# Kernel optimization log

Hardware: AMD Instinct MI355X
Metric: run time of the kernel (lower is better)

The kernel has to match this reference:

```python
import jax, jax.numpy as jnp
import numpy as np

EMB = 768
HS = 64
B, T = 4, 4096


def setup_inputs() -> dict:
    key = jax.random.key(0)
    ks = jax.random.split(key, 7)
    s = 1.0 / np.sqrt(EMB)
    return {
        "x": jax.random.normal(ks[0], (B, T, EMB), dtype=jnp.float32),
        "Wk": jax.random.normal(ks[1], (EMB, HS), dtype=jnp.float32) * s,
        "bk": jnp.zeros((HS,), dtype=jnp.float32),
        "Wq": jax.random.normal(ks[2], (EMB, HS), dtype=jnp.float32) * s,
        "bq": jnp.zeros((HS,), dtype=jnp.float32),
        "Wv": jax.random.normal(ks[3], (EMB, HS), dtype=jnp.float32) * s,
        "bv": jnp.zeros((HS,), dtype=jnp.float32),
    }


def reference(x, Wk, bk, Wq, bq, Wv, bv):
    # Linear projections: (B, T, emb) @ (emb, hs) + bias -> (B, T, hs)
    k = x @ Wk + bk
    q = x @ Wq + bq
    v = x @ Wv + bv
    # NOTE: original code computes key @ query^T (k on the left), no 1/sqrt(hs) scaling.
    att = jnp.einsum("bth,bsh->bts", k, q)  # (B, T, T)
    causal = jnp.tril(jnp.ones((T, T), dtype=bool))  # (T, T)
    att = jnp.where(causal, att, -jnp.inf)
    wei = jax.nn.softmax(att, axis=-1)
    return jnp.einsum("bts,bsh->bth", wei, v)  # (B, T, hs)
```

## Files before the change

kernel.cpp:

```cpp
#include <hip/hip_runtime.h>
#include <cmath>

static constexpr int EMB  = 768;
static constexpr int HS   = 64;
static constexpr int NB   = 4;
static constexpr int SEQ  = 4096;
static constexpr int MTOT = NB * SEQ;
static constexpr int SPLITS = 8;

typedef __attribute__((ext_vector_type(8))) short  short8x;
typedef __attribute__((ext_vector_type(4))) float  float4x;
typedef __attribute__((ext_vector_type(4))) unsigned short ushort4x;

__device__ inline unsigned short rne16(float f) {
    unsigned u = __builtin_bit_cast(unsigned, f);
    unsigned r = u + 0x7FFFu + ((u >> 16) & 1u);
    return (unsigned short)(r >> 16);
}
__device__ inline float bf2f(unsigned short h) {
    return __builtin_bit_cast(float, ((unsigned)h) << 16);
}

__global__ __launch_bounds__(256) void convert_w(
    const float* __restrict__ Wk, const float* __restrict__ Wq, const float* __restrict__ Wv,
    unsigned short* __restrict__ wpk)
{
    const int t    = blockIdx.x * 256 + threadIdx.x;
    const int lane = t & 63;
    const int rest = t >> 6;
    const int nng  = rest % 12;
    const int kcp  = rest / 12;
    const int kc   = kcp % 24;
    const int p    = kcp / 24;
    const int which= nng >> 2;
    const int nn   = nng & 3;
    const float* W = (which == 0) ? Wk : (which == 1) ? Wq : Wv;
    const int col  = nn * 16 + (lane & 15);
    const int kr   = kc * 32 + (lane >> 4) * 8;

    unsigned short o[8];
    #pragma unroll
    for (int j = 0; j < 8; ++j) {
        float w = W[(size_t)(kr + j) * HS + col];
        unsigned short h = rne16(w);
        o[j] = (p == 0) ? h : rne16(w - bf2f(h));
    }
    size_t base = ((size_t)((p * 24 + kc) * 12 + nng) * 64 + lane) * 8;
    *(short8x*)&wpk[base] = *(short8x*)o;
}

__global__ __launch_bounds__(256) void proj_kernel(
    const float* __restrict__ x,
    const unsigned short* __restrict__ wpk,
    const float* __restrict__ bk, const float* __restrict__ bq, const float* __restrict__ bv,
    unsigned short* __restrict__ khi, unsigned short* __restrict__ klo,
    unsigned short* __restrict__ qhi, unsigned short* __restrict__ qlo,
    unsigned short* __restrict__ vT)
{
    __shared__ unsigned short xh[2][32 * 72];
    __shared__ unsigned short xl[2][32 * 72];

    const int tid  = threadIdx.x;
    const int lane = tid & 63;
    const int w    = tid >> 6;
    const int l15  = lane & 15;
    const int quad = lane >> 4;
    const int row0 = blockIdx.x * 32;

    float4x acc[3][2] = {};
    float4  pre[2];

    #pragma unroll
    for (int it = 0; it < 2; ++it) {
        const int fi = tid + it * 256;
        const int r  = fi >> 4, c4 = (fi & 15) * 4;
        pre[it] = *(const float4*)&x[(size_t)(row0 + r) * EMB + 0 * 64 + c4];
    }
    #pragma unroll
    for (int it = 0; it < 2; ++it) {
        const int fi = tid + it * 256;
        const int r  = fi >> 4, c4 = (fi & 15) * 4;
        const float4 xv = pre[it];
        const unsigned short h0 = rne16(xv.x), h1 = rne16(xv.y),
                             h2 = rne16(xv.z), h3 = rne16(xv.w);
        ushort4x hv = {h0, h1, h2, h3};
        ushort4x lv = {rne16(xv.x - bf2f(h0)), rne16(xv.y - bf2f(h1)),
                       rne16(xv.z - bf2f(h2)), rne16(xv.w - bf2f(h3))};
        *(ushort4x*)&xh[0][r * 72 + c4] = hv;
        *(ushort4x*)&xl[0][r * 72 + c4] = lv;
    }

    for (int ch = 0; ch < 12; ++ch) {
        if (ch + 1 < 12) {
            #pragma unroll
            for (int it = 0; it < 2; ++it) {
                const int fi = tid + it * 256;
                const int r  = fi >> 4, c4 = (fi & 15) * 4;
                pre[it] = *(const float4*)&x[(size_t)(row0 + r) * EMB + (ch + 1) * 64 + c4];
            }
        }
        __syncthreads();
        const int buf = ch & 1;

        #pragma unroll
        for (int k0i = 0; k0i < 2; ++k0i) {
            const int k0 = k0i * 32;
            const int kc = ch * 2 + k0i;
            short8x ah[2], al[2];
            #pragma unroll
            for (int mi = 0; mi < 2; ++mi) {
                ah[mi] = *(const short8x*)&xh[buf][(mi * 16 + l15) * 72 + k0 + quad * 8];
                al[mi] = *(const short8x*)&xl[buf][(mi * 16 + l15) * 72 + k0 + quad * 8];
            }
            #pragma unroll
            for (int which = 0; which < 3; ++which) {
                const int nng = which * 4 + w;
                const short8x bh = *(const short8x*)&wpk[((size_t)((0 * 24 + kc) * 12 + nng) * 64 + lane) * 8];
                const short8x bl = *(const short8x*)&wpk[((size_t)((1 * 24 + kc) * 12 + nng) * 64 + lane) * 8];
                #pragma unroll
                for (int mi = 0; mi < 2; ++mi) {
                    acc[which][mi] = __builtin_amdgcn_mfma_f32_16x16x32_bf16(ah[mi], bh, acc[which][mi], 0, 0, 0);
                    acc[which][mi] = __builtin_amdgcn_mfma_f32_16x16x32_bf16(ah[mi], bl, acc[which][mi], 0, 0, 0);
                    acc[which][mi] = __builtin_amdgcn_mfma_f32_16x16x32_bf16(al[mi], bh, acc[which][mi], 0, 0, 0);
                }
            }
        }

        if (ch + 1 < 12) {
            const int nbuf = (ch + 1) & 1;
            #pragma unroll
            for (int it = 0; it < 2; ++it) {
                const int fi = tid + it * 256;
                const int r  = fi >> 4, c4 = (fi & 15) * 4;
                const float4 xv = pre[it];
                const unsigned short h0 = rne16(xv.x), h1 = rne16(xv.y),
                                     h2 = rne16(xv.z), h3 = rne16(xv.w);
                ushort4x hv = {h0, h1, h2, h3};
                ushort4x lv = {rne16(xv.x - bf2f(h0)), rne16(xv.y - bf2f(h1)),
                               rne16(xv.z - bf2f(h2)), rne16(xv.w - bf2f(h3))};
                *(ushort4x*)&xh[nbuf][r * 72 + c4] = hv;
                *(ushort4x*)&xl[nbuf][r * 72 + c4] = lv;
            }
        }
    }

    const int col = w * 16 + l15;
    const float bkv = bk[col], bqv = bq[col], bvv = bv[col];
    #pragma unroll
    for (int mi = 0; mi < 2; ++mi) {
        const int rbase = row0 + mi * 16 + quad * 4;
        #pragma unroll
        for (int r = 0; r < 4; ++r) {
            const float kv = acc[0][mi][r] + bkv;
            const unsigned short hk = rne16(kv);
            khi[(size_t)(rbase + r) * 64 + col] = hk;
            klo[(size_t)(rbase + r) * 64 + col] = rne16(kv - bf2f(hk));
            const float qv = acc[1][mi][r] + bqv;
            const unsigned short hq = rne16(qv);
            qhi[(size_t)(rbase + r) * 64 + col] = hq;
            qlo[(size_t)(rbase + r) * 64 + col] = rne16(qv - bf2f(hq));
        }
        const int b = rbase / SEQ;
        const int s = rbase % SEQ;
        ushort4x vv = {rne16(acc[2][mi][0] + bvv), rne16(acc[2][mi][1] + bvv),
                       rne16(acc[2][mi][2] + bvv), rne16(acc[2][mi][3] + bvv)};
        *(ushort4x*)&vT[((size_t)b * 64 + col) * SEQ + s] = vv;
    }
}

__global__ __launch_bounds__(256, 2) void attn_kernel(
    const unsigned short* __restrict__ khi, const unsigned short* __restrict__ klo,
    const unsigned short* __restrict__ qhi, const unsigned short* __restrict__ qlo,
    const unsigned short* __restrict__ vT,
    float* __restrict__ Opart, float* __restrict__ lpart)
{
    __shared__ unsigned short qh_s[64 * 72];
    __shared__ unsigned short ql_s[64 * 72];
    __shared__ unsigned short vt_s[64 * 72];
    __shared__ unsigned short psH[64 * 72];
    __shared__ unsigned short psL[64 * 72];

    const int tid  = threadIdx.x;
    const int lane = tid & 63;
    const int w    = tid >> 6;
    const int l15  = lane & 15;
    const int quad = lane >> 4;

    const int n  = blockIdx.x;
    const int sp = n & (SPLITS - 1);
    const int b  = (n >> 3) & (NB - 1);
    const int p  = n >> 5;
    const int jj[4] = {63 - p, 32 + p, 31 - p, p};
    const size_t rowb = (size_t)b * SEQ;

    float4x oacc[4][4] = {};
    float   l_r[4][4]  = {};

    const int sr = tid >> 3;
    const int c8 = (tid & 7) * 8;

    for (int ci = sp; ci <= jj[0]; ci += SPLITS) {
        const int s0 = ci * 64;
        __syncthreads();
        #pragma unroll
        for (int it = 0; it < 2; ++it) {
            const int r = sr + it * 32;
            *(short8x*)&qh_s[r * 72 + c8] = *(const short8x*)&qhi[(rowb + s0 + r) * 64 + c8];
            *(short8x*)&ql_s[r * 72 + c8] = *(const short8x*)&qlo[(rowb + s0 + r) * 64 + c8];
            *(short8x*)&vt_s[r * 72 + c8] = *(const short8x*)&vT[((size_t)b * 64 + r) * SEQ + s0 + c8];
        }
        __syncthreads();

        #pragma unroll
        for (int g = 0; g < 2; ++g) {
            const int idxH = g ? 1 : 0;
            const int idxL = g ? 2 : 3;
            const int jH = jj[idxH], jL = jj[idxL];
            const bool aH = (ci <= jH), aL = (ci <= jL);
            if (!aH && !aL) continue;

            short8x ahH[2], alH[2], ahL[2], alL[2];
            #pragma unroll
            for (int k0 = 0; k0 < 2; ++k0) {
                if (aH) {
                    const size_t rH = (rowb + jH * 64 + 16 * w + l15) * 64 + k0 * 32 + quad * 8;
                    ahH[k0] = *(const short8x*)&khi[rH];
                    alH[k0] = *(const short8x*)&klo[rH];
                }
                if (aL) {
                    const size_t rL = (rowb + jL * 64 + 16 * w + l15) * 64 + k0 * 32 + quad * 8;
                    ahL[k0] = *(const short8x*)&khi[rL];
                    alL[k0] = *(const short8x*)&klo[rL];
                }
            }

            float4x sH[4] = {}, sL[4] = {};
            #pragma unroll
            for (int k0 = 0; k0 < 2; ++k0) {
                #pragma unroll
                for (int nn = 0; nn < 4; ++nn) {
                    const short8x bh = *(const short8x*)&qh_s[(nn * 16 + l15) * 72 + k0 * 32 + quad * 8];
                    const short8x bl = *(const short8x*)&ql_s[(nn * 16 + l15) * 72 + k0 * 32 + quad * 8];
                    if (aH) {
                        sH[nn] = __builtin_amdgcn_mfma_f32_16x16x32_bf16(ahH[k0], bh, sH[nn], 0, 0, 0);
                        sH[nn] = __builtin_amdgcn_mfma_f32_16x16x32_bf16(alH[k0], bh, sH[nn], 0, 0, 0);
                        sH[nn] = __builtin_amdgcn_mfma_f32_16x16x32_bf16(ahH[k0], bl, sH[nn], 0, 0, 0);
                    }
                    if (aL) {
                        sL[nn] = __builtin_amdgcn_mfma_f32_16x16x32_bf16(ahL[k0], bh, sL[nn], 0, 0, 0);
                        sL[nn] = __builtin_amdgcn_mfma_f32_16x16x32_bf16(alL[k0], bh, sL[nn], 0, 0, 0);
                        sL[nn] = __builtin_amdgcn_mfma_f32_16x16x32_bf16(ahL[k0], bl, sL[nn], 0, 0, 0);
                    }
                }
            }

            #pragma unroll
            for (int hl = 0; hl < 2; ++hl) {
                const bool alive = hl ? aL : aH;
                if (!alive) continue;
                const int j   = hl ? jL : jH;
                const int idx = hl ? idxL : idxH;
                float4x* sc   = hl ? sL : sH;
                unsigned short* ps = hl ? psL : psH;
                if (ci == j) {
                    const int trow = j * 64 + 16 * w + quad * 4;
                    #pragma unroll
                    for (int nn = 0; nn < 4; ++nn) {
                        const int colg = s0 + nn * 16 + l15;
                        #pragma unroll
                        for (int r = 0; r < 4; ++r)
                            if (colg > trow + r) sc[nn][r] = -1e30f;
                    }
                }
                #pragma unroll
                for (int nn = 0; nn < 4; ++nn) {
                    #pragma unroll
                    for (int r = 0; r < 4; ++r) {
                        const float e = __expf(fminf(sc[nn][r], 80.0f));
                        const unsigned short h = rne16(e);
                        l_r[idx][r] += bf2f(h);
                        ps[(16 * w + quad * 4 + r) * 72 + nn * 16 + l15] = h;
                    }
                }
            }

            #pragma unroll
            for (int k0 = 0; k0 < 2; ++k0) {
                short8x paH, paL;
                if (aH) paH = *(const short8x*)&psH[(16 * w + l15) * 72 + k0 * 32 + quad * 8];
                if (aL) paL = *(const short8x*)&psL[(16 * w + l15) * 72 + k0 * 32 + quad * 8];
                #pragma unroll
                for (int nn = 0; nn < 4; ++nn) {
                    const short8x vb = *(const short8x*)&vt_s[(nn * 16 + l15) * 72 + k0 * 32 + quad * 8];
                    if (aH) oacc[idxH][nn] = __builtin_amdgcn_mfma_f32_16x16x32_bf16(paH, vb, oacc[idxH][nn], 0, 0, 0);
                    if (aL) oacc[idxL][nn] = __builtin_amdgcn_mfma_f32_16x16x32_bf16(paL, vb, oacc[idxL][nn], 0, 0, 0);
                }
            }
        }
    }

    #pragma unroll
    for (int idx = 0; idx < 4; ++idx) {
        const int j = jj[idx];
        if (idx == 3 && sp > p) continue;
        float lv[4];
        #pragma unroll
        for (int r = 0; r < 4; ++r) {
            float l = l_r[idx][r];
            l += __shfl_xor(l, 1);
            l += __shfl_xor(l, 2);
            l += __shfl_xor(l, 4);
            l += __shfl_xor(l, 8);
            lv[r] = l;
        }
        const size_t part = (size_t)(j * NB + b) * SPLITS + sp;
        float* Op = Opart + part * 4096;
        #pragma unroll
        for (int nn = 0; nn < 4; ++nn)
            #pragma unroll
            for (int r = 0; r < 4; ++r)
                Op[(16 * w + quad * 4 + r) * 64 + nn * 16 + l15] = oacc[idx][nn][r];
        if (l15 == 0) {
            #pragma unroll
            for (int r = 0; r < 4; ++r)
                lpart[part * 64 + 16 * w + quad * 4 + r] = lv[r];
        }
    }
}

__global__ __launch_bounds__(256) void combine_kernel(
    const float* __restrict__ Opart, const float* __restrict__ lpart,
    float* __restrict__ out)
{
    const int j   = blockIdx.x;
    const int b   = blockIdx.y;
    const int tid = threadIdx.x;
    const int row = tid >> 2;
    const int c0  = (tid & 3) * 16;
    const size_t base = (size_t)(j * NB + b) * SPLITS;

    float4 acc[4] = {};
    float lsum = 0.f;
    for (int sp = 0; sp < SPLITS; ++sp) {
        const float l = lpart[(base + sp) * 64 + row];
        if (l > 0.f) {
            lsum += l;
            const float* Op = Opart + (base + sp) * 4096 + row * 64 + c0;
            #pragma unroll
            for (int u = 0; u < 4; ++u) {
                const float4 v = *(const float4*)&Op[u * 4];
                acc[u].x += v.x; acc[u].y += v.y; acc[u].z += v.z; acc[u].w += v.w;
            }
        }
    }
    const float inv = 1.0f / lsum;
    float* o = out + ((size_t)b * SEQ + j * 64 + row) * 64 + c0;
    #pragma unroll
    for (int u = 0; u < 4; ++u) {
        float4 v;
        v.x = acc[u].x * inv; v.y = acc[u].y * inv;
        v.z = acc[u].z * inv; v.w = acc[u].w * inv;
        *(float4*)&o[u * 4] = v;
    }
}

extern "C" void kernel_launch(void* const* d_in, const int* in_sizes, int n_in,
                              void* d_out, int out_size, void* d_ws, size_t ws_size,
                              hipStream_t stream)
{
    const float* x  = (const float*)d_in[0];
    const float* Wk = (const float*)d_in[1];
    const float* bk = (const float*)d_in[2];
    const float* Wq = (const float*)d_in[3];
    const float* bq = (const float*)d_in[4];
    const float* Wv = (const float*)d_in[5];
    const float* bv = (const float*)d_in[6];
    float* out = (float*)d_out;

    const size_t NE = (size_t)MTOT * HS;
    unsigned short* khi = (unsigned short*)d_ws;
    unsigned short* klo = khi + NE;
    unsigned short* qhi = klo + NE;
    unsigned short* qlo = qhi + NE;
    unsigned short* vT  = qlo + NE;
    unsigned short* wpk = vT + NE;
    float* Opart = (float*)(wpk + 294912);
    float* lpart = Opart + (size_t)64 * NB * SPLITS * 4096;

    hipMemsetAsync(lpart, 0, (size_t)64 * NB * SPLITS * 64 * sizeof(float), stream);
    convert_w<<<144, 256, 0, stream>>>(Wk, Wq, Wv, wpk);
    proj_kernel<<<MTOT / 32, 256, 0, stream>>>(x, wpk, bk, bq, bv, khi, klo, qhi, qlo, vT);
    attn_kernel<<<16 * NB * SPLITS, 256, 0, stream>>>(khi, klo, qhi, qlo, vT, Opart, lpart);
    dim3 cgrid(64, NB);
    combine_kernel<<<cgrid, 256, 0, stream>>>(Opart, lpart, out);
}
```

Baseline: 160.6 us.

## Raise attention split count, store normalized bf16 partials, shrink projection tiles

The attention kernel now uses a runtime split count, 16 by default and dropping to 8 if the workspace is too small, doubling the grid to improve load balance and occupancy across CUs. Partial outputs are normalized per split and stored as bf16, halving partial-output traffic. The combine kernel reweights them by each split's l. The two P staging buffers merge into one to cut LDS and allow 4 blocks per CU, and the projection kernel uses 16-row tiles with doubled grid. Storing partials in bf16 costs output precision, and more splits add combine work.

After: 224.9 us. 1.4x slower.

```diff
diff --git a/kernel.cpp b/kernel.cpp
--- a/kernel.cpp
+++ b/kernel.cpp
@@ -6,7 +6,6 @@
 static constexpr int NB   = 4;
 static constexpr int SEQ  = 4096;
 static constexpr int MTOT = NB * SEQ;
-static constexpr int SPLITS = 8;
 
 typedef __attribute__((ext_vector_type(8))) short  short8x;
 typedef __attribute__((ext_vector_type(4))) float  float4x;
@@ -49,7 +48,7 @@
     *(short8x*)&wpk[base] = *(short8x*)o;
 }
 
-__global__ __launch_bounds__(256) void proj_kernel(
+__global__ __launch_bounds__(256, 4) void proj_kernel(
     const float* __restrict__ x,
     const unsigned short* __restrict__ wpk,
     const float* __restrict__ bk, const float* __restrict__ bq, const float* __restrict__ bv,
@@ -57,48 +56,37 @@
     unsigned short* __restrict__ qhi, unsigned short* __restrict__ qlo,
     unsigned short* __restrict__ vT)
 {
-    __shared__ unsigned short xh[2][32 * 72];
-    __shared__ unsigned short xl[2][32 * 72];
+    __shared__ unsigned short xh[2][16 * 72];
+    __shared__ unsigned short xl[2][16 * 72];
 
     const int tid  = threadIdx.x;
     const int lane = tid & 63;
     const int w    = tid >> 6;
     const int l15  = lane & 15;
     const int quad = lane >> 4;
-    const int row0 = blockIdx.x * 32;
-
-    float4x acc[3][2] = {};
-    float4  pre[2];
-
-    #pragma unroll
-    for (int it = 0; it < 2; ++it) {
-        const int fi = tid + it * 256;
-        const int r  = fi >> 4, c4 = (fi & 15) * 4;
-        pre[it] = *(const float4*)&x[(size_t)(row0 + r) * EMB + 0 * 64 + c4];
-    }
-    #pragma unroll
-    for (int it = 0; it < 2; ++it) {
-        const int fi = tid + it * 256;
-        const int r  = fi >> 4, c4 = (fi & 15) * 4;
-        const float4 xv = pre[it];
+    const int row0 = blockIdx.x * 16;
+
+    const int s_r  = tid >> 4;
+    const int s_c4 = (tid & 15) * 4;
+
+    float4x acc[3] = {};
+    float4  pre;
+
+    pre = *(const float4*)&x[(size_t)(row0 + s_r) * EMB + 0 * 64 + s_c4];
+    {
+        const float4 xv = pre;
         const unsigned short h0 = rne16(xv.x), h1 = rne16(xv.y),
                              h2 = rne16(xv.z), h3 = rne16(xv.w);
         ushort4x hv = {h0, h1, h2, h3};
         ushort4x lv = {rne16(xv.x - bf2f(h0)), rne16(xv.y - bf2f(h1)),
                        rne16(xv.z - bf2f(h2)), rne16(xv.w - bf2f(h3))};
-        *(ushort4x*)&xh[0][r * 72 + c4] = hv;
-        *(ushort4x*)&xl[0][r * 72 + c4] = lv;
+        *(ushort4x*)&xh[0][s_r * 72 + s_c4] = hv;
+        *(ushort4x*)&xl[0][s_r * 72 + s_c4] = lv;
     }
 
     for (int ch = 0; ch < 12; ++ch) {
-        if (ch + 1 < 12) {
-            #pragma unroll
-            for (int it = 0; it < 2; ++it) {
-                const int fi = tid + it * 256;
-                const int r  = fi >> 4, c4 = (fi & 15) * 4;
-                pre[it] = *(const float4*)&x[(size_t)(row0 + r) * EMB + (ch + 1) * 64 + c4];
-            }
-        }
+        if (ch + 1 < 12)
+            pre = *(const float4*)&x[(size_t)(row0 + s_r) * EMB + (ch + 1) * 64 + s_c4];
         __syncthreads();
         const int buf = ch & 1;
 
@@ -106,79 +94,63 @@
         for (int k0i = 0; k0i < 2; ++k0i) {
             const int k0 = k0i * 32;
             const int kc = ch * 2 + k0i;
-            short8x ah[2], al[2];
-            #pragma unroll
-            for (int mi = 0; mi < 2; ++mi) {
-                ah[mi] = *(const short8x*)&xh[buf][(mi * 16 + l15) * 72 + k0 + quad * 8];
-                al[mi] = *(const short8x*)&xl[buf][(mi * 16 + l15) * 72 + k0 + quad * 8];
-            }
+            const short8x ah = *(const short8x*)&xh[buf][l15 * 72 + k0 + quad * 8];
+            const short8x al = *(const short8x*)&xl[buf][l15 * 72 + k0 + quad * 8];
             #pragma unroll
             for (int which = 0; which < 3; ++which) {
                 const int nng = which * 4 + w;
                 const short8x bh = *(const short8x*)&wpk[((size_t)((0 * 24 + kc) * 12 + nng) * 64 + lane) * 8];
                 const short8x bl = *(const short8x*)&wpk[((size_t)((1 * 24 + kc) * 12 + nng) * 64 + lane) * 8];
-                #pragma unroll
-                for (int mi = 0; mi < 2; ++mi) {
-                    acc[which][mi] = __builtin_amdgcn_mfma_f32_16x16x32_bf16(ah[mi], bh, acc[which][mi], 0, 0, 0);
-                    acc[which][mi] = __builtin_amdgcn_mfma_f32_16x16x32_bf16(ah[mi], bl, acc[which][mi], 0, 0, 0);
-                    acc[which][mi] = __builtin_amdgcn_mfma_f32_16x16x32_bf16(al[mi], bh, acc[which][mi], 0, 0, 0);
-                }
+                acc[which] = __builtin_amdgcn_mfma_f32_16x16x32_bf16(ah, bh, acc[which], 0, 0, 0);
+                acc[which] = __builtin_amdgcn_mfma_f32_16x16x32_bf16(ah, bl, acc[which], 0, 0, 0);
+                acc[which] = __builtin_amdgcn_mfma_f32_16x16x32_bf16(al, bh, acc[which], 0, 0, 0);
             }
         }
 
         if (ch + 1 < 12) {
             const int nbuf = (ch + 1) & 1;
-            #pragma unroll
-            for (int it = 0; it < 2; ++it) {
-                const int fi = tid + it * 256;
-                const int r  = fi >> 4, c4 = (fi & 15) * 4;
-                const float4 xv = pre[it];
-                const unsigned short h0 = rne16(xv.x), h1 = rne16(xv.y),
-                                     h2 = rne16(xv.z), h3 = rne16(xv.w);
-                ushort4x hv = {h0, h1, h2, h3};
-                ushort4x lv = {rne16(xv.x - bf2f(h0)), rne16(xv.y - bf2f(h1)),
-                               rne16(xv.z - bf2f(h2)), rne16(xv.w - bf2f(h3))};
-                *(ushort4x*)&xh[nbuf][r * 72 + c4] = hv;
-                *(ushort4x*)&xl[nbuf][r * 72 + c4] = lv;
-            }
+            const float4 xv = pre;
+            const unsigned short h0 = rne16(xv.x), h1 = rne16(xv.y),
+                                 h2 = rne16(xv.z), h3 = rne16(xv.w);
+            ushort4x hv = {h0, h1, h2, h3};
+            ushort4x lv = {rne16(xv.x - bf2f(h0)), rne16(xv.y - bf2f(h1)),
+                           rne16(xv.z - bf2f(h2)), rne16(xv.w - bf2f(h3))};
+            *(ushort4x*)&xh[nbuf][s_r * 72 + s_c4] = hv;
+            *(ushort4x*)&xl[nbuf][s_r * 72 + s_c4] = lv;
         }
     }
 
     const int col = w * 16 + l15;
     const float bkv = bk[col], bqv = bq[col], bvv = bv[col];
+    const int rbase = row0 + quad * 4;
     #pragma unroll
-    for (int mi = 0; mi < 2; ++mi) {
-        const int rbase = row0 + mi * 16 + quad * 4;
-        #pragma unroll
-        for (int r = 0; r < 4; ++r) {
-            const float kv = acc[0][mi][r] + bkv;
-            const unsigned short hk = rne16(kv);
-            khi[(size_t)(rbase + r) * 64 + col] = hk;
-            klo[(size_t)(rbase + r) * 64 + col] = rne16(kv - bf2f(hk));
-            const float qv = acc[1][mi][r] + bqv;
-            const unsigned short hq = rne16(qv);
-            qhi[(size_t)(rbase + r) * 64 + col] = hq;
-            qlo[(size_t)(rbase + r) * 64 + col] = rne16(qv - bf2f(hq));
-        }
-        const int b = rbase / SEQ;
-        const int s = rbase % SEQ;
-        ushort4x vv = {rne16(acc[2][mi][0] + bvv), rne16(acc[2][mi][1] + bvv),
-                       rne16(acc[2][mi][2] + bvv), rne16(acc[2][mi][3] + bvv)};
-        *(ushort4x*)&vT[((size_t)b * 64 + col) * SEQ + s] = vv;
-    }
-}
-
-__global__ __launch_bounds__(256, 2) void attn_kernel(
+    for (int r = 0; r < 4; ++r) {
+        const float kv = acc[0][r] + bkv;
+        const unsigned short hk = rne16(kv);
+        khi[(size_t)(rbase + r) * 64 + col] = hk;
+        klo[(size_t)(rbase + r) * 64 + col] = rne16(kv - bf2f(hk));
+        const float qv = acc[1][r] + bqv;
+        const unsigned short hq = rne16(qv);
+        qhi[(size_t)(rbase + r) * 64 + col] = hq;
+        qlo[(size_t)(rbase + r) * 64 + col] = rne16(qv - bf2f(hq));
+    }
+    const int b = rbase / SEQ;
+    const int s = rbase % SEQ;
+    ushort4x vv = {rne16(acc[2][0] + bvv), rne16(acc[2][1] + bvv),
+                   rne16(acc[2][2] + bvv), rne16(acc[2][3] + bvv)};
+    *(ushort4x*)&vT[((size_t)b * 64 + col) * SEQ + s] = vv;
+}
+
+__global__ __launch_bounds__(256, 4) void attn_kernel(
     const unsigned short* __restrict__ khi, const unsigned short* __restrict__ klo,
     const unsigned short* __restrict__ qhi, const unsigned short* __restrict__ qlo,
     const unsigned short* __restrict__ vT,
-    float* __restrict__ Opart, float* __restrict__ lpart)
+    unsigned short* __restrict__ Opart, float* __restrict__ lpart, int S)
 {
     __shared__ unsigned short qh_s[64 * 72];
     __shared__ unsigned short ql_s[64 * 72];
     __shared__ unsigned short vt_s[64 * 72];
-    __shared__ unsigned short psH[64 * 72];
-    __shared__ unsigned short psL[64 * 72];
+    __shared__ unsigned short ps[64 * 72];
 
     const int tid  = threadIdx.x;
     const int lane = tid & 63;
@@ -186,10 +158,11 @@
     const int l15  = lane & 15;
     const int quad = lane >> 4;
 
-    const int n  = blockIdx.x;
-    const int sp = n & (SPLITS - 1);
-    const int b  = (n >> 3) & (NB - 1);
-    const int p  = n >> 5;
+    const int n    = blockIdx.x;
+    const int sp   = n % S;
+    const int rest = n / S;
+    const int b    = rest & (NB - 1);
+    const int p    = rest >> 2;
     const int jj[4] = {63 - p, 32 + p, 31 - p, p};
     const size_t rowb = (size_t)b * SEQ;
 
@@ -199,7 +172,7 @@
     const int sr = tid >> 3;
     const int c8 = (tid & 7) * 8;
 
-    for (int ci = sp; ci <= jj[0]; ci += SPLITS) {
+    for (int ci = sp; ci <= jj[0]; ci += S) {
         const int s0 = ci * 64;
         __syncthreads();
         #pragma unroll
@@ -261,7 +234,6 @@
                 const int j   = hl ? jL : jH;
                 const int idx = hl ? idxL : idxH;
                 float4x* sc   = hl ? sL : sH;
-                unsigned short* ps = hl ? psL : psH;
                 if (ci == j) {
                     const int trow = j * 64 + 16 * w + quad * 4;
                     #pragma unroll
@@ -282,18 +254,14 @@
                         ps[(16 * w + quad * 4 + r) * 72 + nn * 16 + l15] = h;
                     }
                 }
-            }
-
-            #pragma unroll
-            for (int k0 = 0; k0 < 2; ++k0) {
-                short8x paH, paL;
-                if (aH) paH = *(const short8x*)&psH[(16 * w + l15) * 72 + k0 * 32 + quad * 8];
-                if (aL) paL = *(const short8x*)&psL[(16 * w + l15) * 72 + k0 * 32 + quad * 8];
                 #pragma unroll
-                for (int nn = 0; nn < 4; ++nn) {
-                    const short8x vb = *(const short8x*)&vt_s[(nn * 16 + l15) * 72 + k0 * 32 + quad * 8];
-                    if (aH) oacc[idxH][nn] = __builtin_amdgcn_mfma_f32_16x16x32_bf16(paH, vb, oacc[idxH][nn], 0, 0, 0);
-                    if (aL) oacc[idxL][nn] = __builtin_amdgcn_mfma_f32_16x16x32_bf16(paL, vb, oacc[idxL][nn], 0, 0, 0);
+                for (int k0 = 0; k0 < 2; ++k0) {
+                    const short8x pa = *(const short8x*)&ps[(16 * w + l15) * 72 + k0 * 32 + quad * 8];
+                    #pragma unroll
+                    for (int nn = 0; nn < 4; ++nn) {
+                        const short8x vb = *(const short8x*)&vt_s[(nn * 16 + l15) * 72 + k0 * 32 + quad * 8];
+                        oacc[idx][nn] = __builtin_amdgcn_mfma_f32_16x16x32_bf16(pa, vb, oacc[idx][nn], 0, 0, 0);
+                    }
                 }
             }
         }
@@ -302,8 +270,7 @@
     #pragma unroll
     for (int idx = 0; idx < 4; ++idx) {
         const int j = jj[idx];
-        if (idx == 3 && sp > p) continue;
-        float lv[4];
+        float lv[4], inv[4];
         #pragma unroll
         for (int r = 0; r < 4; ++r) {
             float l = l_r[idx][r];
@@ -311,15 +278,16 @@
             l += __shfl_xor(l, 2);
             l += __shfl_xor(l, 4);
             l += __shfl_xor(l, 8);
-            lv[r] = l;
-        }
-        const size_t part = (size_t)(j * NB + b) * SPLITS + sp;
-        float* Op = Opart + part * 4096;
+            lv[r]  = l;
+            inv[r] = (l > 0.f) ? 1.0f / l : 0.0f;
+        }
+        const size_t part = (size_t)(j * NB + b) * S + sp;
+        unsigned short* Op = Opart + part * 4096;
         #pragma unroll
         for (int nn = 0; nn < 4; ++nn)
             #pragma unroll
             for (int r = 0; r < 4; ++r)
-                Op[(16 * w + quad * 4 + r) * 64 + nn * 16 + l15] = oacc[idx][nn][r];
+                Op[(16 * w + quad * 4 + r) * 64 + nn * 16 + l15] = rne16(oacc[idx][nn][r] * inv[r]);
         if (l15 == 0) {
             #pragma unroll
             for (int r = 0; r < 4; ++r)
@@ -329,28 +297,28 @@
 }
 
 __global__ __launch_bounds__(256) void combine_kernel(
-    const float* __restrict__ Opart, const float* __restrict__ lpart,
-    float* __restrict__ out)
+    const unsigned short* __restrict__ Opart, const float* __restrict__ lpart,
+    float* __restrict__ out, int S)
 {
     const int j   = blockIdx.x;
     const int b   = blockIdx.y;
     const int tid = threadIdx.x;
     const int row = tid >> 2;
     const int c0  = (tid & 3) * 16;
-    const size_t base = (size_t)(j * NB + b) * SPLITS;
-
-    float4 acc[4] = {};
+    const size_t base = (size_t)(j * NB + b) * S;
+
+    float acc[16] = {};
     float lsum = 0.f;
-    for (int sp = 0; sp < SPLITS; ++sp) {
+    for (int sp = 0; sp < S; ++sp) {
         const float l = lpart[(base + sp) * 64 + row];
-        if (l > 0.f) {
-            lsum += l;
-            const float* Op = Opart + (base + sp) * 4096 + row * 64 + c0;
-            #pragma unroll
-            for (int u = 0; u < 4; ++u) {
-                const float4 v = *(const float4*)&Op[u * 4];
-                acc[u].x += v.x; acc[u].y += v.y; acc[u].z += v.z; acc[u].w += v.w;
-            }
+        lsum += l;
+        const unsigned short* Op = Opart + (base + sp) * 4096 + row * 64 + c0;
+        const short8x v0 = *(const short8x*)&Op[0];
+        const short8x v1 = *(const short8x*)&Op[8];
+        #pragma unroll
+        for (int u = 0; u < 8; ++u) {
+            acc[u]     += l * bf2f((unsigned short)v0[u]);
+            acc[u + 8] += l * bf2f((unsigned short)v1[u]);
         }
     }
     const float inv = 1.0f / lsum;
@@ -358,8 +326,8 @@
     #pragma unroll
     for (int u = 0; u < 4; ++u) {
         float4 v;
-        v.x = acc[u].x * inv; v.y = acc[u].y * inv;
-        v.z = acc[u].z * inv; v.w = acc[u].w * inv;
+        v.x = acc[u * 4 + 0] * inv; v.y = acc[u * 4 + 1] * inv;
+        v.z = acc[u * 4 + 2] * inv; v.w = acc[u * 4 + 3] * inv;
         *(float4*)&o[u * 4] = v;
     }
 }
@@ -384,13 +352,21 @@
     unsigned short* qlo = qhi + NE;
     unsigned short* vT  = qlo + NE;
     unsigned short* wpk = vT + NE;
-    float* Opart = (float*)(wpk + 294912);
-    float* lpart = Opart + (size_t)64 * NB * SPLITS * 4096;
-
-    hipMemsetAsync(lpart, 0, (size_t)64 * NB * SPLITS * 64 * sizeof(float), stream);
+    const size_t fixed_bytes = 5 * NE * sizeof(unsigned short) + 294912 * sizeof(unsigned short);
+
+    int S = 16;
+    while (S > 8) {
+        const size_t need = fixed_bytes +
+            (size_t)64 * NB * S * (4096 * sizeof(unsigned short) + 64 * sizeof(float));
+        if (need <= ws_size) break;
+        S >>= 1;
+    }
+    unsigned short* Opart = wpk + 294912;
+    float* lpart = (float*)(Opart + (size_t)64 * NB * S * 4096);
+
     convert_w<<<144, 256, 0, stream>>>(Wk, Wq, Wv, wpk);
-    proj_kernel<<<MTOT / 32, 256, 0, stream>>>(x, wpk, bk, bq, bv, khi, klo, qhi, qlo, vT);
-    attn_kernel<<<16 * NB * SPLITS, 256, 0, stream>>>(khi, klo, qhi, qlo, vT, Opart, lpart);
+    proj_kernel<<<MTOT / 16, 256, 0, stream>>>(x, wpk, bk, bq, bv, khi, klo, qhi, qlo, vT);
+    attn_kernel<<<16 * NB * S, 256, 0, stream>>>(khi, klo, qhi, qlo, vT, Opart, lpart, S);
     dim3 cgrid(64, NB);
-    combine_kernel<<<cgrid, 256, 0, stream>>>(Opart, lpart, out);
-}
+    combine_kernel<<<cgrid, 256, 0, stream>>>(Opart, lpart, out, S);
+}
```
